# Optimization experiments

Measured on AMD Instinct MI355X. Metric: run time of the kernel, lower is better.

The kernel has to match this reference:

```python
import jax, jax.numpy as jnp
import numpy as np

B, L, H = 2, 2048, 1024
NH, KVH = 16, 4
HD = H // NH          # 64
G = NH // KVH         # 4 query heads per kv head


def setup_inputs() -> dict:
    key = jax.random.key(0)
    ks = jax.random.split(key, 10)
    s = 0.02
    return {
        "hidden_states": jax.random.normal(ks[0], (B, L, H), dtype=jnp.float32),
        "attention_mask": jnp.zeros((B, 1, L, L), dtype=jnp.float32),
        "Wq": jax.random.normal(ks[1], (H, H), dtype=jnp.float32) * s,
        "bq": jnp.zeros((H,), dtype=jnp.float32),
        "Wk": jax.random.normal(ks[2], (KVH * HD, H), dtype=jnp.float32) * s,
        "bk": jnp.zeros((KVH * HD,), dtype=jnp.float32),
        "Wv": jax.random.normal(ks[3], (KVH * HD, H), dtype=jnp.float32) * s,
        "bv": jnp.zeros((KVH * HD,), dtype=jnp.float32),
        "Wo": jax.random.normal(ks[4], (H, H), dtype=jnp.float32) * s,
        "bo": jnp.zeros((H,), dtype=jnp.float32),
    }


def reference(hidden_states, attention_mask, Wq, bq, Wk, bk, Wv, bv, Wo, bo):
    x = hidden_states
    # projections (torch Linear: x @ W.T + b)
    q = (x @ Wq.T + bq).reshape(B, L, NH, HD).transpose(0, 2, 1, 3)   # [B,NH,L,HD]
    k = (x @ Wk.T + bk).reshape(B, L, KVH, HD).transpose(0, 2, 1, 3)  # [B,KVH,L,HD]
    v = (x @ Wv.T + bv).reshape(B, L, KVH, HD).transpose(0, 2, 1, 3)
    # GQA: group query heads per kv head instead of repeat_interleave (same math)
    qg = q.reshape(B, KVH, G, L, HD)
    scores = jnp.einsum("bkgqd,bkld->bkgql", qg, k) / jnp.sqrt(jnp.float32(HD))
    scores = scores + attention_mask[:, :, None, :, :]  # mask broadcasts over heads
    attn = jax.nn.softmax(scores, axis=-1)              # dropout p=0 -> identity
    ctx = jnp.einsum("bkgql,bkld->bkgqd", attn, v)      # [B,KVH,G,L,HD]
    ctx = ctx.reshape(B, NH, L, HD).transpose(0, 2, 1, 3).reshape(B, L, H)
    return ctx @ Wo.T + bo
```

## Files before the change

kernel.cpp:

```cpp
#include <hip/hip_runtime.h>

#define B_   2
#define L_   2048
#define H_   1024
#define NH_  16
#define KVH_ 4
#define HD_  64

typedef short short8 __attribute__((ext_vector_type(8)));
typedef float f32x4 __attribute__((ext_vector_type(4)));
typedef float f32x16 __attribute__((ext_vector_type(16)));
typedef unsigned short u16x4 __attribute__((ext_vector_type(4)));

#define LOG2E 1.4426950408889634f
#define QSC   0.18033688011112042f
#define MFMA   __builtin_amdgcn_mfma_f32_16x16x32_bf16
#define MFMA32 __builtin_amdgcn_mfma_f32_32x32x16_bf16

#if __has_builtin(__builtin_amdgcn_exp2f)
#define EXP2(x) __builtin_amdgcn_exp2f(x)
#else
#define EXP2(x) exp2f(x)
#endif

static __device__ __forceinline__ unsigned short f2bf(float f) {
  unsigned int u = __float_as_uint(f);
  u += 0x7FFFu + ((u >> 16) & 1u);
  return (unsigned short)(u >> 16);
}

static __device__ __forceinline__ unsigned int cvtpk(float lo, float hi) {
  unsigned int r;
  asm("v_cvt_pk_bf16_f32 %0, %1, %2" : "=v"(r) : "v"(lo), "v"(hi));
  return r;
}

static __device__ __forceinline__ void plswap(unsigned int& a, unsigned int& b) {
  asm("v_permlane32_swap_b32 %0, %1" : "+v"(a), "+v"(b));
}

static __device__ __forceinline__ short8 mk8(unsigned int w0, unsigned int w1,
                                             unsigned int w2, unsigned int w3) {
  union { unsigned int u[4]; short8 s; } x;
  x.u[0] = w0; x.u[1] = w1; x.u[2] = w2; x.u[3] = w3;
  return x.s;
}

static __device__ __forceinline__ void gload_lds16(const void* g, void* l) {
  __builtin_amdgcn_global_load_lds(
      (const __attribute__((address_space(1))) unsigned int*)g,
      (__attribute__((address_space(3))) unsigned int*)l, 16, 0, 0);
}

__global__ __launch_bounds__(256) void k_prep(const float* __restrict__ x,
                                              const float* __restrict__ Wq,
                                              const float* __restrict__ Wk,
                                              const float* __restrict__ Wv,
                                              const float* __restrict__ Wo,
                                              const float* __restrict__ mask,
                                              unsigned short* __restrict__ xb,
                                              unsigned short* __restrict__ wcat,
                                              unsigned short* __restrict__ wo_b,
                                              unsigned char* __restrict__ flags) {
  const int blk = blockIdx.x;
  const int t = threadIdx.x;
  if (blk < 4096) {
    size_t i = ((size_t)blk * 256 + t) * 4;
    float4 v = *(const float4*)(x + i);
    u16x4 o = { f2bf(v.x), f2bf(v.y), f2bf(v.z), f2bf(v.w) };
    *(u16x4*)(xb + i) = o;
  } else if (blk < 6656) {
    int r = blk - 4096;
    int c = t * 4;
    const float* src;
    unsigned short* dst;
    if (r < 1024)      { src = Wq + (size_t)r * 1024;          dst = wcat + (size_t)r * 1024; }
    else if (r < 1280) { src = Wk + (size_t)(r - 1024) * 1024; dst = wcat + (size_t)r * 1024; }
    else if (r < 1536) { src = Wv + (size_t)(r - 1280) * 1024; dst = wcat + (size_t)r * 1024; }
    else               { src = Wo + (size_t)(r - 1536) * 1024; dst = wo_b + (size_t)(r - 1536) * 1024; }
    float4 v = *(const float4*)(src + c);
    u16x4 o = { f2bf(v.x), f2bf(v.y), f2bf(v.z), f2bf(v.w) };
    *(u16x4*)(dst + c) = o;
  } else {
    const int mb = blk - 6656;
    const int b = mb >> 10, qb = (mb >> 5) & 31, kb = mb & 31;
    const float* base = mask + ((size_t)b * L_ + qb * 64) * L_ + kb * 64;
    const int r0 = t >> 4, c = (t & 15) * 4;
    bool nz = false;
#pragma unroll
    for (int i = 0; i < 4; ++i) {
      float4 v = *(const float4*)(base + (size_t)(r0 + i * 16) * L_ + c);
      nz |= (v.x != 0.f) | (v.y != 0.f) | (v.z != 0.f) | (v.w != 0.f);
    }
    __shared__ int anyv;
    if (t == 0) anyv = 0;
    __syncthreads();
    if (__any(nz) && (t & 63) == 0) atomicOr(&anyv, 1);
    __syncthreads();
    if (t == 0) flags[mb] = (unsigned char)anyv;
  }
}

template <int MODE>
__global__ __launch_bounds__(256) void k_gemm(const unsigned short* __restrict__ A,
                                              const unsigned short* __restrict__ Bt,
                                              const float* __restrict__ bias0,
                                              const float* __restrict__ bias1,
                                              const float* __restrict__ bias2,
                                              unsigned short* __restrict__ q_ws,
                                              unsigned short* __restrict__ k_ws,
                                              unsigned short* __restrict__ vt_ws,
                                              float* __restrict__ outp) {
  const int bn = blockIdx.x, bm = blockIdx.y;
  const int t = threadIdx.x;
  const int lane = t & 63, li = lane & 15, g = lane >> 4;
  const int wid = t >> 6, wr = wid >> 1, wc = wid & 1;
  __shared__ unsigned short lds_a[128 * 64];
  __shared__ unsigned short lds_b[128 * 64];

  const f32x4 z = {0.f, 0.f, 0.f, 0.f};
  f32x4 acc[4][4];
#pragma unroll
  for (int m = 0; m < 4; ++m)
#pragma unroll
    for (int n = 0; n < 4; ++n) acc[m][n] = z;

  const unsigned short* asrc[4];
  const unsigned short* bsrc[4];
  int ldst[4];
#pragma unroll
  for (int c = 0; c < 4; ++c) {
    const int idx = c * 256 + t, row = idx >> 3, sl = idx & 7;
    const int gcol = (sl ^ (row & 7)) * 8;
    asrc[c] = A  + (size_t)(bm * 128 + row) * 1024 + gcol;
    bsrc[c] = Bt + (size_t)(bn * 128 + row) * 1024 + gcol;
    ldst[c] = idx * 8;
  }
  const int rs = li & 7;

  for (int kt = 0; kt < 1024; kt += 64) {
#pragma unroll
    for (int c = 0; c < 4; ++c) {
      gload_lds16(asrc[c] + kt, &lds_a[ldst[c]]);
      gload_lds16(bsrc[c] + kt, &lds_b[ldst[c]]);
    }
    __syncthreads();
#pragma unroll
    for (int ks = 0; ks < 2; ++ks) {
      short8 af[4], bf[4];
#pragma unroll
      for (int m = 0; m < 4; ++m)
        af[m] = *(const short8*)&lds_a[(wr * 64 + m * 16 + li) * 64 + (((ks * 4 + g) ^ rs) * 8)];
#pragma unroll
      for (int n = 0; n < 4; ++n)
        bf[n] = *(const short8*)&lds_b[(wc * 64 + n * 16 + li) * 64 + (((ks * 4 + g) ^ rs) * 8)];
#pragma unroll
      for (int m = 0; m < 4; ++m)
#pragma unroll
        for (int n = 0; n < 4; ++n)
          acc[m][n] = MFMA(af[m], bf[n], acc[m][n], 0, 0, 0);
    }
    __syncthreads();
  }

#pragma unroll
  for (int m = 0; m < 4; ++m) {
    const int row0 = bm * 128 + wr * 64 + m * 16 + 4 * g;
#pragma unroll
    for (int n = 0; n < 4; ++n) {
      const int col = bn * 128 + wc * 64 + n * 16 + li;
      f32x4 v = acc[m][n];
      if (MODE == 1) {
        const float bias = bias0[col];
#pragma unroll
        for (int r = 0; r < 4; ++r) outp[(size_t)(row0 + r) * 1024 + col] = v[r] + bias;
      } else {
        if (col < 1024) {
          const float bias = bias0[col];
#pragma unroll
          for (int r = 0; r < 4; ++r) q_ws[(size_t)(row0 + r) * 1024 + col] = f2bf((v[r] + bias) * QSC);
        } else if (col < 1280) {
          const int cc = col - 1024;
          const float bias = bias1[cc];
#pragma unroll
          for (int r = 0; r < 4; ++r) k_ws[(size_t)(row0 + r) * 256 + cc] = f2bf(v[r] + bias);
        } else {
          const int cc = col - 1280;
          const float bias = bias2[cc];
          const int kvh = cc >> 6, d = cc & 63;
          const int b = row0 >> 11, l0 = row0 & 2047;
          u16x4 pk = { f2bf(v[0] + bias), f2bf(v[1] + bias), f2bf(v[2] + bias), f2bf(v[3] + bias) };
          *(u16x4*)(vt_ws + ((size_t)((b * KVH_ + kvh) * 64 + d)) * 2048 + l0) = pk;
        }
      }
    }
  }
}

__global__ __launch_bounds__(512, 4) void k_attn(const unsigned short* __restrict__ q_ws,
                                                 const unsigned short* __restrict__ k_ws,
                                                 const unsigned short* __restrict__ vt_ws,
                                                 const float* __restrict__ mask,
                                                 const unsigned char* __restrict__ mflags,
                                                 unsigned short* __restrict__ ctx) {
  const int bk = blockIdx.x;
  const int qt = blockIdx.y;
  const int b = bk >> 2, kvh = bk & 3;
  const int t = threadIdx.x;
  const int wid = t >> 6, lane = t & 63;
  const int l31 = lane & 31, g1 = lane >> 5;
  const int h = wid & 3, kh = wid >> 2;

  __shared__ unsigned short smem[16384];
  __shared__ float lred[4][64];

  const unsigned short* qbase = q_ws + ((size_t)b * L_ + qt * 32 + l31) * H_ +
                                (kvh * 4 + h) * 64 + g1 * 8;
  short8 qf[4];
#pragma unroll
  for (int ks = 0; ks < 4; ++ks) qf[ks] = *(const short8*)(qbase + ks * 16);

  const unsigned int* fp = (const unsigned int*)(mflags + b * 1024 + (qt >> 1) * 32);
  unsigned int fm = 0;
#pragma unroll
  for (int w = 0; w < 8; ++w) {
    unsigned int wv = fp[w];
    fm |= ((wv & 0x000000FFu) ? 1u : 0u) << (w * 4 + 0);
    fm |= ((wv & 0x0000FF00u) ? 1u : 0u) << (w * 4 + 1);
    fm |= ((wv & 0x00FF0000u) ? 1u : 0u) << (w * 4 + 2);
    fm |= ((wv & 0xFF000000u) ? 1u : 0u) << (w * 4 + 3);
  }
  fm = __builtin_amdgcn_readfirstlane(fm);

  const int srow = t >> 3, sgr = t & 7;
  const int swz = (sgr ^ (srow & 7)) * 8;
  const unsigned short* ksrc = k_ws + ((size_t)b * L_ + srow) * 256 + kvh * 64 + swz;
  const unsigned short* vsrc = vt_ws + ((size_t)(b * KVH_ + kvh) * 64 + srow) * 2048 + swz;

  const f32x16 z16 = {0,0,0,0,0,0,0,0,0,0,0,0,0,0,0,0};
  f32x16 o_[2];
  o_[0] = z16; o_[1] = z16;
  float l_part = 0.f;

  const int rK = kh * 32 + l31, swK = rK & 7;
  const int swV = l31 & 7;

  short8 kst, vst;
#define LOADR(kt) { kst = *(const short8*)(ksrc + (size_t)(kt) * 16384); \
                    vst = *(const short8*)(vsrc + (kt) * 64); }
#define WRITES(buf) { unsigned short* dk = smem + (buf) * 8192;          \
                      *(short8*)(dk + t * 8) = kst;                      \
                      *(short8*)(dk + 4096 + t * 8) = vst; }

  LOADR(0);
  WRITES(0);
  LOADR(1);
  __syncthreads();

#pragma unroll 1
  for (int kt = 0; kt < 32; ++kt) {
    const int cur = kt & 1;
    const unsigned short* lk = smem + cur * 8192;
    const unsigned short* lv = lk + 4096;

    short8 kf[4];
#pragma unroll
    for (int ks = 0; ks < 4; ++ks)
      kf[ks] = *(const short8*)&lk[rK * 64 + ((ks * 2 + g1) ^ swK) * 8];
    short8 vf[2][2];
#pragma unroll
    for (int db = 0; db < 2; ++db)
#pragma unroll
      for (int s = 0; s < 2; ++s)
        vf[db][s] = *(const short8*)&lv[(db * 32 + l31) * 64 + ((kh * 4 + s * 2 + g1) ^ swV) * 8];

    asm volatile("s_waitcnt vmcnt(0)" ::: "memory");
    if (kt + 1 < 32) WRITES(cur ^ 1);
    if (kt + 2 < 32) LOADR(kt + 2);

    f32x16 sv = z16;
    __builtin_amdgcn_s_setprio(1);
#pragma unroll
    for (int ks = 0; ks < 4; ++ks) sv = MFMA32(kf[ks], qf[ks], sv, 0, 0, 0);
    __builtin_amdgcn_s_setprio(0);

    if (fm & (1u << kt)) {
      const float* mrow = mask + ((size_t)b * L_ + qt * 32 + l31) * L_ + kt * 64 + kh * 32 + g1 * 4;
#pragma unroll
      for (int rg = 0; rg < 4; ++rg) {
        float4 mv = *(const float4*)(mrow + rg * 8);
#pragma unroll
        for (int j = 0; j < 4; ++j) sv[rg * 4 + j] = fmaf((&mv.x)[j], LOG2E, sv[rg * 4 + j]);
      }
    }

    float e[16];
#pragma unroll
    for (int r = 0; r < 16; ++r) e[r] = EXP2(sv[r]);
    l_part += (((e[0] + e[1]) + (e[2] + e[3])) + ((e[4] + e[5]) + (e[6] + e[7]))) +
              (((e[8] + e[9]) + (e[10] + e[11])) + ((e[12] + e[13]) + (e[14] + e[15])));
    unsigned int w0 = cvtpk(e[0], e[1]),   w1 = cvtpk(e[2], e[3]);
    unsigned int w2 = cvtpk(e[4], e[5]),   w3 = cvtpk(e[6], e[7]);
    unsigned int w4 = cvtpk(e[8], e[9]),   w5 = cvtpk(e[10], e[11]);
    unsigned int w6 = cvtpk(e[12], e[13]), w7 = cvtpk(e[14], e[15]);
    plswap(w0, w2); plswap(w1, w3);
    plswap(w4, w6); plswap(w5, w7);
    short8 pa0 = mk8(w0, w1, w2, w3);
    short8 pa1 = mk8(w4, w5, w6, w7);

    __builtin_amdgcn_s_setprio(1);
#pragma unroll
    for (int db = 0; db < 2; ++db) {
      o_[db] = MFMA32(vf[db][0], pa0, o_[db], 0, 0, 0);
      o_[db] = MFMA32(vf[db][1], pa1, o_[db], 0, 0, 0);
    }
    __builtin_amdgcn_s_setprio(0);

    asm volatile("s_waitcnt lgkmcnt(0)" ::: "memory");
    __builtin_amdgcn_s_barrier();
    __builtin_amdgcn_sched_barrier(0);
  }
#undef LOADR
#undef WRITES

  float lt = l_part + __shfl_xor(l_part, 32);
  float* red = (float*)smem;

  if (kh == 1) {
    lred[h][lane] = lt;
#pragma unroll
    for (int db = 0; db < 2; ++db)
#pragma unroll
      for (int w4 = 0; w4 < 4; ++w4) {
        f32x4 pv = { o_[db][w4 * 4 + 0], o_[db][w4 * 4 + 1],
                     o_[db][w4 * 4 + 2], o_[db][w4 * 4 + 3] };
        *(f32x4*)&red[(((h * 2 + db) * 4 + w4) * 64 + lane) * 4] = pv;
      }
  }
  __syncthreads();

  if (kh == 0) {
    const float inv = 1.f / (lt + lred[h][lane]);
#pragma unroll
    for (int db = 0; db < 2; ++db) {
      f32x16 acc = o_[db];
#pragma unroll
      for (int w4 = 0; w4 < 4; ++w4) {
        f32x4 pv = *(const f32x4*)&red[(((h * 2 + db) * 4 + w4) * 64 + lane) * 4];
#pragma unroll
        for (int j = 0; j < 4; ++j) acc[w4 * 4 + j] += pv[j];
      }
      unsigned short* cp = ctx + ((size_t)b * L_ + qt * 32 + l31) * H_ +
                           (kvh * 4 + h) * 64 + db * 32 + g1 * 4;
#pragma unroll
      for (int k4 = 0; k4 < 4; ++k4) {
        unsigned int a0 = cvtpk(acc[4 * k4 + 0] * inv, acc[4 * k4 + 1] * inv);
        unsigned int a1 = cvtpk(acc[4 * k4 + 2] * inv, acc[4 * k4 + 3] * inv);
        *(unsigned int*)(cp + 8 * k4) = a0;
        *(unsigned int*)(cp + 8 * k4 + 2) = a1;
      }
    }
  }
}

extern "C" void kernel_launch(void* const* d_in, const int* in_sizes, int n_in,
                              void* d_out, int out_size, void* d_ws, size_t ws_size,
                              hipStream_t stream) {
  const float* x    = (const float*)d_in[0];
  const float* mask = (const float*)d_in[1];
  const float* Wq   = (const float*)d_in[2];
  const float* bq   = (const float*)d_in[3];
  const float* Wk   = (const float*)d_in[4];
  const float* bk   = (const float*)d_in[5];
  const float* Wv   = (const float*)d_in[6];
  const float* bv   = (const float*)d_in[7];
  const float* Wo   = (const float*)d_in[8];
  const float* bo   = (const float*)d_in[9];
  float* out = (float*)d_out;

  char* ws = (char*)d_ws;
  unsigned short* xb    = (unsigned short*)(ws);
  unsigned short* ctx   = xb;
  unsigned short* wcat  = (unsigned short*)(ws + 8388608);
  unsigned short* wo_b  = (unsigned short*)(ws + 11534336);
  unsigned short* q_ws  = (unsigned short*)(ws + 13631488);
  unsigned short* k_ws  = (unsigned short*)(ws + 22020096);
  unsigned short* vt_ws = (unsigned short*)(ws + 24117248);
  unsigned char*  mflg  = (unsigned char*)(ws + 26214400);

  k_prep<<<dim3(8704), dim3(256), 0, stream>>>(x, Wq, Wk, Wv, Wo, mask, xb, wcat, wo_b, mflg);
  k_gemm<0><<<dim3(12, 32), dim3(256), 0, stream>>>(xb, wcat, bq, bk, bv, q_ws, k_ws, vt_ws, nullptr);
  k_attn<<<dim3(8, 64), dim3(512), 0, stream>>>(q_ws, k_ws, vt_ws, mask, mflg, ctx);
  k_gemm<1><<<dim3(8, 32), dim3(256), 0, stream>>>(ctx, wo_b, bo, nullptr, nullptr,
                                                   nullptr, nullptr, nullptr, out);
}
```

Baseline: 106.5 us.

## Double query rows per attention block, each wave handling two heads

The attention kernel now covers 64 query rows per block instead of 32. Each wave computes two query heads against the same K/V fragments loaded from shared memory, so every K/V tile staged in LDS feeds twice as many MFMAs and the grid is halved. The cost is more accumulator and query registers per thread: launch bounds drop to 2 blocks per CU, and the final cross-wave reduction now runs in two phases with an extra barrier.

```diff
diff --git a/kernel.cpp b/kernel.cpp
--- a/kernel.cpp
+++ b/kernel.cpp
@@ -197,7 +197,7 @@
   }
 }
 
-__global__ __launch_bounds__(512, 4) void k_attn(const unsigned short* __restrict__ q_ws,
+__global__ __launch_bounds__(512, 2) void k_attn(const unsigned short* __restrict__ q_ws,
                                                  const unsigned short* __restrict__ k_ws,
                                                  const unsigned short* __restrict__ vt_ws,
                                                  const float* __restrict__ mask,
@@ -209,18 +209,23 @@
   const int t = threadIdx.x;
   const int wid = t >> 6, lane = t & 63;
   const int l31 = lane & 31, g1 = lane >> 5;
-  const int h = wid & 3, kh = wid >> 2;
+  const int hp = wid & 1, qh = (wid >> 1) & 1, kh = wid >> 2;
 
   __shared__ unsigned short smem[16384];
-  __shared__ float lred[4][64];
-
-  const unsigned short* qbase = q_ws + ((size_t)b * L_ + qt * 32 + l31) * H_ +
-                                (kvh * 4 + h) * 64 + g1 * 8;
-  short8 qf[4];
-#pragma unroll
-  for (int ks = 0; ks < 4; ++ks) qf[ks] = *(const short8*)(qbase + ks * 16);
-
-  const unsigned int* fp = (const unsigned int*)(mflags + b * 1024 + (qt >> 1) * 32);
+  __shared__ float lred[4][2][64];
+
+  const int qrow = qt * 64 + qh * 32 + l31;
+
+  const unsigned short* qbase = q_ws + ((size_t)b * L_ + qrow) * H_ +
+                                (kvh * 4 + hp * 2) * 64 + g1 * 8;
+  short8 qf[2][4];
+#pragma unroll
+  for (int h2 = 0; h2 < 2; ++h2)
+#pragma unroll
+    for (int ks = 0; ks < 4; ++ks)
+      qf[h2][ks] = *(const short8*)(qbase + h2 * 64 + ks * 16);
+
+  const unsigned int* fp = (const unsigned int*)(mflags + b * 1024 + qt * 32);
   unsigned int fm = 0;
 #pragma unroll
   for (int w = 0; w < 8; ++w) {
@@ -238,9 +243,10 @@
   const unsigned short* vsrc = vt_ws + ((size_t)(b * KVH_ + kvh) * 64 + srow) * 2048 + swz;
 
   const f32x16 z16 = {0,0,0,0,0,0,0,0,0,0,0,0,0,0,0,0};
-  f32x16 o_[2];
-  o_[0] = z16; o_[1] = z16;
-  float l_part = 0.f;
+  f32x16 o_[4];
+#pragma unroll
+  for (int i = 0; i < 4; ++i) o_[i] = z16;
+  float l_part[2] = {0.f, 0.f};
 
   const int rK = kh * 32 + l31, swK = rK & 7;
   const int swV = l31 & 7;
@@ -278,42 +284,56 @@
     if (kt + 1 < 32) WRITES(cur ^ 1);
     if (kt + 2 < 32) LOADR(kt + 2);
 
-    f32x16 sv = z16;
+    f32x16 sv[2];
+    sv[0] = z16; sv[1] = z16;
     __builtin_amdgcn_s_setprio(1);
 #pragma unroll
-    for (int ks = 0; ks < 4; ++ks) sv = MFMA32(kf[ks], qf[ks], sv, 0, 0, 0);
+    for (int ks = 0; ks < 4; ++ks) {
+      sv[0] = MFMA32(kf[ks], qf[0][ks], sv[0], 0, 0, 0);
+      sv[1] = MFMA32(kf[ks], qf[1][ks], sv[1], 0, 0, 0);
+    }
     __builtin_amdgcn_s_setprio(0);
 
     if (fm & (1u << kt)) {
-      const float* mrow = mask + ((size_t)b * L_ + qt * 32 + l31) * L_ + kt * 64 + kh * 32 + g1 * 4;
+      const float* mrow = mask + ((size_t)b * L_ + qrow) * L_ + kt * 64 + kh * 32 + g1 * 4;
 #pragma unroll
       for (int rg = 0; rg < 4; ++rg) {
         float4 mv = *(const float4*)(mrow + rg * 8);
 #pragma unroll
-        for (int j = 0; j < 4; ++j) sv[rg * 4 + j] = fmaf((&mv.x)[j], LOG2E, sv[rg * 4 + j]);
+        for (int j = 0; j < 4; ++j) {
+          const float mj = (&mv.x)[j] * LOG2E;
+          sv[0][rg * 4 + j] += mj;
+          sv[1][rg * 4 + j] += mj;
+        }
       }
     }
 
-    float e[16];
-#pragma unroll
-    for (int r = 0; r < 16; ++r) e[r] = EXP2(sv[r]);
-    l_part += (((e[0] + e[1]) + (e[2] + e[3])) + ((e[4] + e[5]) + (e[6] + e[7]))) +
-              (((e[8] + e[9]) + (e[10] + e[11])) + ((e[12] + e[13]) + (e[14] + e[15])));
-    unsigned int w0 = cvtpk(e[0], e[1]),   w1 = cvtpk(e[2], e[3]);
-    unsigned int w2 = cvtpk(e[4], e[5]),   w3 = cvtpk(e[6], e[7]);
-    unsigned int w4 = cvtpk(e[8], e[9]),   w5 = cvtpk(e[10], e[11]);
-    unsigned int w6 = cvtpk(e[12], e[13]), w7 = cvtpk(e[14], e[15]);
-    plswap(w0, w2); plswap(w1, w3);
-    plswap(w4, w6); plswap(w5, w7);
-    short8 pa0 = mk8(w0, w1, w2, w3);
-    short8 pa1 = mk8(w4, w5, w6, w7);
+    short8 pa[2][2];
+#pragma unroll
+    for (int h2 = 0; h2 < 2; ++h2) {
+      float e[16];
+#pragma unroll
+      for (int r = 0; r < 16; ++r) e[r] = EXP2(sv[h2][r]);
+      l_part[h2] += (((e[0] + e[1]) + (e[2] + e[3])) + ((e[4] + e[5]) + (e[6] + e[7]))) +
+                    (((e[8] + e[9]) + (e[10] + e[11])) + ((e[12] + e[13]) + (e[14] + e[15])));
+      unsigned int w0 = cvtpk(e[0], e[1]),   w1 = cvtpk(e[2], e[3]);
+      unsigned int w2 = cvtpk(e[4], e[5]),   w3 = cvtpk(e[6], e[7]);
+      unsigned int w4 = cvtpk(e[8], e[9]),   w5 = cvtpk(e[10], e[11]);
+      unsigned int w6 = cvtpk(e[12], e[13]), w7 = cvtpk(e[14], e[15]);
+      plswap(w0, w2); plswap(w1, w3);
+      plswap(w4, w6); plswap(w5, w7);
+      pa[h2][0] = mk8(w0, w1, w2, w3);
+      pa[h2][1] = mk8(w4, w5, w6, w7);
+    }
 
     __builtin_amdgcn_s_setprio(1);
 #pragma unroll
-    for (int db = 0; db < 2; ++db) {
-      o_[db] = MFMA32(vf[db][0], pa0, o_[db], 0, 0, 0);
-      o_[db] = MFMA32(vf[db][1], pa1, o_[db], 0, 0, 0);
-    }
+    for (int h2 = 0; h2 < 2; ++h2)
+#pragma unroll
+      for (int db = 0; db < 2; ++db) {
+        o_[h2 * 2 + db] = MFMA32(vf[db][0], pa[h2][0], o_[h2 * 2 + db], 0, 0, 0);
+        o_[h2 * 2 + db] = MFMA32(vf[db][1], pa[h2][1], o_[h2 * 2 + db], 0, 0, 0);
+      }
     __builtin_amdgcn_s_setprio(0);
 
     asm volatile("s_waitcnt lgkmcnt(0)" ::: "memory");
@@ -323,41 +343,51 @@
 #undef LOADR
 #undef WRITES
 
-  float lt = l_part + __shfl_xor(l_part, 32);
+  float lt[2];
+  lt[0] = l_part[0] + __shfl_xor(l_part[0], 32);
+  lt[1] = l_part[1] + __shfl_xor(l_part[1], 32);
   float* red = (float*)smem;
+  const int wq = hp * 2 + qh;
 
   if (kh == 1) {
-    lred[h][lane] = lt;
-#pragma unroll
-    for (int db = 0; db < 2; ++db)
-#pragma unroll
-      for (int w4 = 0; w4 < 4; ++w4) {
-        f32x4 pv = { o_[db][w4 * 4 + 0], o_[db][w4 * 4 + 1],
-                     o_[db][w4 * 4 + 2], o_[db][w4 * 4 + 3] };
-        *(f32x4*)&red[(((h * 2 + db) * 4 + w4) * 64 + lane) * 4] = pv;
-      }
-  }
-  __syncthreads();
-
-  if (kh == 0) {
-    const float inv = 1.f / (lt + lred[h][lane]);
-#pragma unroll
-    for (int db = 0; db < 2; ++db) {
-      f32x16 acc = o_[db];
-#pragma unroll
-      for (int w4 = 0; w4 < 4; ++w4) {
-        f32x4 pv = *(const f32x4*)&red[(((h * 2 + db) * 4 + w4) * 64 + lane) * 4];
-#pragma unroll
-        for (int j = 0; j < 4; ++j) acc[w4 * 4 + j] += pv[j];
-      }
-      unsigned short* cp = ctx + ((size_t)b * L_ + qt * 32 + l31) * H_ +
-                           (kvh * 4 + h) * 64 + db * 32 + g1 * 4;
-#pragma unroll
-      for (int k4 = 0; k4 < 4; ++k4) {
-        unsigned int a0 = cvtpk(acc[4 * k4 + 0] * inv, acc[4 * k4 + 1] * inv);
-        unsigned int a1 = cvtpk(acc[4 * k4 + 2] * inv, acc[4 * k4 + 3] * inv);
-        *(unsigned int*)(cp + 8 * k4) = a0;
-        *(unsigned int*)(cp + 8 * k4 + 2) = a1;
+    lred[wq][0][lane] = lt[0];
+    lred[wq][1][lane] = lt[1];
+  }
+
+#pragma unroll
+  for (int h2 = 0; h2 < 2; ++h2) {
+    if (h2 == 1) __syncthreads();
+    if (kh == 1) {
+#pragma unroll
+      for (int db = 0; db < 2; ++db)
+#pragma unroll
+        for (int w4 = 0; w4 < 4; ++w4) {
+          f32x4 pv = { o_[h2 * 2 + db][w4 * 4 + 0], o_[h2 * 2 + db][w4 * 4 + 1],
+                       o_[h2 * 2 + db][w4 * 4 + 2], o_[h2 * 2 + db][w4 * 4 + 3] };
+          *(f32x4*)&red[(((wq * 2 + db) * 4 + w4) * 64 + lane) * 4] = pv;
+        }
+    }
+    __syncthreads();
+    if (kh == 0) {
+      const float inv = 1.f / (lt[h2] + lred[wq][h2][lane]);
+#pragma unroll
+      for (int db = 0; db < 2; ++db) {
+        f32x16 acc = o_[h2 * 2 + db];
+#pragma unroll
+        for (int w4 = 0; w4 < 4; ++w4) {
+          f32x4 pv = *(const f32x4*)&red[(((wq * 2 + db) * 4 + w4) * 64 + lane) * 4];
+#pragma unroll
+          for (int j = 0; j < 4; ++j) acc[w4 * 4 + j] += pv[j];
+        }
+        unsigned short* cp = ctx + ((size_t)b * L_ + qrow) * H_ +
+                             (kvh * 4 + hp * 2 + h2) * 64 + db * 32 + g1 * 4;
+#pragma unroll
+        for (int k4 = 0; k4 < 4; ++k4) {
+          unsigned int a0 = cvtpk(acc[4 * k4 + 0] * inv, acc[4 * k4 + 1] * inv);
+          unsigned int a1 = cvtpk(acc[4 * k4 + 2] * inv, acc[4 * k4 + 3] * inv);
+          *(unsigned int*)(cp + 8 * k4) = a0;
+          *(unsigned int*)(cp + 8 * k4 + 2) = a1;
+        }
       }
     }
   }
@@ -390,7 +420,7 @@
 
   k_prep<<<dim3(8704), dim3(256), 0, stream>>>(x, Wq, Wk, Wv, Wo, mask, xb, wcat, wo_b, mflg);
   k_gemm<0><<<dim3(12, 32), dim3(256), 0, stream>>>(xb, wcat, bq, bk, bv, q_ws, k_ws, vt_ws, nullptr);
-  k_attn<<<dim3(8, 64), dim3(512), 0, stream>>>(q_ws, k_ws, vt_ws, mask, mflg, ctx);
+  k_attn<<<dim3(8, 32), dim3(512), 0, stream>>>(q_ws, k_ws, vt_ws, mask, mflg, ctx);
   k_gemm<1><<<dim3(8, 32), dim3(256), 0, stream>>>(ctx, wo_b, bo, nullptr, nullptr,
                                                    nullptr, nullptr, nullptr, out);
 }
```

Measured after the change: 107.6 us. Within noise of the previous version (+1.0%).
